# Kernel optimization log

Measured on AMD Instinct MI355X. Metric: run time of the kernel, lower is better.

Reference implementation:

```python
import math
import jax
import jax.numpy as jnp
import numpy as np

WH, WW = 8, 8
DIM, NUM_HEADS = 768, 24
CPB_HIDDEN = 512


def _rel_tables(Wh, Ww):
    # relative_position_index: (N, N) int, values in [0, (2Wh-1)*(2Ww-1))
    coords = np.stack(np.meshgrid(np.arange(Wh), np.arange(Ww), indexing='ij')).reshape(2, -1)
    rel = coords[:, :, None] - coords[:, None, :]          # (2, N, N)
    rel = rel.transpose(1, 2, 0).astype(np.int64)          # (N, N, 2)
    rel[:, :, 0] += Wh - 1
    rel[:, :, 1] += Ww - 1
    rel[:, :, 0] *= 2 * Ww - 1
    idx = rel.sum(-1)                                      # (N, N)
    # relative_coords_table: ((2Wh-1)*(2Ww-1), 2), log-spaced CPB coords
    rch = np.arange(-(Wh - 1), Wh, dtype=np.float32)
    rcw = np.arange(-(Ww - 1), Ww, dtype=np.float32)
    table = np.stack(np.meshgrid(rch, rcw, indexing='ij')).transpose(1, 2, 0).reshape(-1, 2)
    table[:, 0] /= max(Wh - 1, 1)
    table[:, 1] /= max(Ww - 1, 1)
    table *= 8.0
    table = np.sign(table) * np.log2(np.abs(table) + 1.0) / math.log2(8.0)
    return idx.astype(np.int32), table.astype(np.float32)


def setup_inputs() -> dict:
    key = jax.random.key(0)
    ks = jax.random.split(key, 8)
    B_, N, C = 1024, WH * WW, DIM
    idx, table = _rel_tables(WH, WW)
    return {
        'x': jax.random.normal(ks[0], (B_, N, C), dtype=jnp.float32),
        'qkv_w': jax.random.normal(ks[1], (C, 3 * C), dtype=jnp.float32) * 0.02,
        'qkv_b': jnp.zeros((3 * C,), dtype=jnp.float32),
        'proj_w': jax.random.normal(ks[2], (C, C), dtype=jnp.float32) * 0.02,
        'proj_b': jnp.zeros((C,), dtype=jnp.float32),
        'cpb_w1': jax.random.normal(ks[3], (2, CPB_HIDDEN), dtype=jnp.float32) * 0.1,
        'cpb_b1': jnp.zeros((CPB_HIDDEN,), dtype=jnp.float32),
        'cpb_w2': jax.random.normal(ks[4], (CPB_HIDDEN, NUM_HEADS), dtype=jnp.float32) * 0.05,
        'logit_scale': jnp.full((NUM_HEADS, 1, 1), math.log(10.0), dtype=jnp.float32),
        'rel_coords_table': jnp.asarray(table),
        'rel_pos_index': jnp.asarray(idx),
    }


def reference(x, qkv_w, qkv_b, proj_w, proj_b, cpb_w1, cpb_b1, cpb_w2,
              logit_scale, rel_coords_table, rel_pos_index):
    B_, N, C = x.shape
    H = logit_scale.shape[0]
    hd = C // H
    qkv = (x @ qkv_w + qkv_b).reshape(B_, N, 3, H, hd).transpose(2, 0, 3, 1, 4)
    q, k, v = qkv[0], qkv[1], qkv[2]                        # (B_, H, N, hd)
    # cosine attention: L2-normalize q, k (eps as in F.normalize)
    q = q / jnp.maximum(jnp.linalg.norm(q, axis=-1, keepdims=True), 1e-12)
    k = k / jnp.maximum(jnp.linalg.norm(k, axis=-1, keepdims=True), 1e-12)
    ls = jnp.exp(jnp.minimum(logit_scale, math.log(1.0 / 0.01)))  # (H,1,1)
    q = q * ls
    # CPB bias: MLP over rel coords table, gather by relative_position_index
    bias_table = jnp.maximum(rel_coords_table @ cpb_w1 + cpb_b1, 0.0) @ cpb_w2  # (T, H)
    bias = bias_table[rel_pos_index.reshape(-1)].reshape(N, N, H).transpose(2, 0, 1)[None]  # (1,H,N,N)
    attn = jnp.einsum('bhnd,bhmd->bhnm', q, k) + bias      # scale = 1.0
    attn = jax.nn.softmax(attn, axis=-1)
    out = jnp.einsum('bhnm,bhmd->bhnd', attn, v)
    out = out.transpose(0, 2, 1, 3).reshape(B_, N, C)
    return out @ proj_w + proj_b
```

## Files before the change

kernel.cpp:

```cpp
#include <hip/hip_runtime.h>
#include <hip/hip_bf16.h>

typedef __bf16 bf16_t;
typedef __bf16 bf16x8 __attribute__((ext_vector_type(8)));
typedef float f32x4 __attribute__((ext_vector_type(4)));

static __device__ __forceinline__ f32x4 mfma16(bf16x8 a, bf16x8 b, f32x4 c) {
  return __builtin_amdgcn_mfma_f32_16x16x32_bf16(a, b, c, 0, 0, 0);
}

static __device__ __forceinline__ void gload16(const void* g, void* l) {
  __builtin_amdgcn_global_load_lds(
      (const __attribute__((address_space(1))) void*)g,
      (__attribute__((address_space(3))) void*)l, 16, 0, 0);
}

#define BAR() __builtin_amdgcn_s_barrier()
#define SCHED0() __builtin_amdgcn_sched_barrier(0)
#define MEMFENCE() asm volatile("" ::: "memory")
#define BARF() do { BAR(); MEMFENCE(); SCHED0(); } while (0)
#define WAITVM4() do { asm volatile("s_waitcnt vmcnt(4)" ::: "memory"); SCHED0(); } while (0)
#define WAITVM0() do { asm volatile("s_waitcnt vmcnt(0)" ::: "memory"); SCHED0(); } while (0)
#define WAITLGKM0() do { asm volatile("s_waitcnt lgkmcnt(0)" ::: "memory"); SCHED0(); } while (0)
#define SP1 __builtin_amdgcn_s_setprio(1)
#define SP0 __builtin_amdgcn_s_setprio(0)

__global__ __launch_bounds__(256) void cvt_bf16_kernel(
    const float* __restrict__ in, bf16_t* __restrict__ out, int n8) {
  int i = blockIdx.x * 256 + threadIdx.x;
  int stride = gridDim.x * 256;
  for (; i < n8; i += stride) {
    float4 a = ((const float4*)in)[2 * i];
    float4 b = ((const float4*)in)[2 * i + 1];
    bf16x8 w = {(bf16_t)a.x, (bf16_t)a.y, (bf16_t)a.z, (bf16_t)a.w,
                (bf16_t)b.x, (bf16_t)b.y, (bf16_t)b.z, (bf16_t)b.w};
    ((bf16x8*)out)[i] = w;
  }
}

__global__ __launch_bounds__(256) void transpose_cvt_kernel(
    const float* __restrict__ W, bf16_t* __restrict__ WT, int K, int N) {
  __shared__ float tile[32][33];
  int n0 = blockIdx.x * 32, k0 = blockIdx.y * 32;
  int tx = threadIdx.x & 31, ty = threadIdx.x >> 5;
#pragma unroll
  for (int i = 0; i < 32; i += 8)
    tile[ty + i][tx] = W[(size_t)(k0 + ty + i) * N + n0 + tx];
  __syncthreads();
#pragma unroll
  for (int i = 0; i < 32; i += 8)
    WT[(size_t)(n0 + ty + i) * K + k0 + tx] = (bf16_t)tile[tx][ty + i];
}

__global__ __launch_bounds__(512) void cpb_table_kernel(
    const float* __restrict__ table, const float* __restrict__ w1,
    const float* __restrict__ b1, const float* __restrict__ w2,
    float* __restrict__ bias_table) {
  __shared__ float hbuf[512];
  int t = blockIdx.x;
  int j = threadIdx.x;
  float c0 = table[2 * t], c1 = table[2 * t + 1];
  float h = c0 * w1[j] + c1 * w1[512 + j] + b1[j];
  hbuf[j] = h > 0.f ? h : 0.f;
  __syncthreads();
  int wave = j >> 6, lane = j & 63;
  for (int hh = wave * 3; hh < wave * 3 + 3; ++hh) {
    float s = 0.f;
    for (int jj = lane; jj < 512; jj += 64) s += hbuf[jj] * w2[jj * 24 + hh];
    for (int off = 32; off > 0; off >>= 1) s += __shfl_down(s, off, 64);
    if (lane == 0) bias_table[t * 24 + hh] = s;
  }
}

__global__ __launch_bounds__(256) void bias_expand_kernel(
    const float* __restrict__ bias_table, const int* __restrict__ idx,
    float* __restrict__ bias) {
  int h = blockIdx.x;
  for (int nm = threadIdx.x; nm < 4096; nm += 256)
    bias[h * 4096 + nm] = bias_table[idx[nm] * 24 + h];
}

template <int EPI, int NCOLS, int K>
__global__ __launch_bounds__(512, 2) void gemm_kernel(
    const bf16_t* __restrict__ A, const bf16_t* __restrict__ BT,
    const float* __restrict__ bias, void* __restrict__ outp) {
  constexpr int NT = NCOLS / 256;
  constexpr int Kb = K * 2;
  constexpr int nk = K / 64;
  constexpr int nIt = nk / 2;
  __shared__ __align__(16) char lds[131072];
  int tid = threadIdx.x;
  int wave = tid >> 6, lane = tid & 63;
  int wm = wave >> 2, wn = wave & 3;
  int cpx = gridDim.x >> 3;
  int wg = (blockIdx.x & 7) * cpx + (blockIdx.x >> 3);
  int mt = wg / NT, nt = wg % NT;
  int m0 = mt * 256, n0 = nt * 256;

  int srow = tid >> 3;
  int sbc = ((tid & 7) << 4) ^ ((srow & 7) << 4);
  const char* Ag = (const char*)A + (size_t)(m0 + srow) * Kb + sbc;
  const char* Bg = (const char*)BT + (size_t)(n0 + srow) * Kb + sbc;
  char* Al = lds + tid * 16;
  char* Bl = lds + 65536 + tid * 16;

#define ST_A(B_, H_, KT_)                                                     \
  do {                                                                        \
    gload16(Ag + (size_t)((H_) * 128) * Kb + (KT_) * 128,                     \
            Al + (B_) * 32768 + (H_) * 16384);                                \
    gload16(Ag + (size_t)((H_) * 128 + 64) * Kb + (KT_) * 128,                \
            Al + (B_) * 32768 + (H_) * 16384 + 8192);                         \
  } while (0)
#define ST_B(B_, H_, KT_)                                                     \
  do {                                                                        \
    gload16(Bg + (size_t)((H_) * 128) * Kb + (KT_) * 128,                     \
            Bl + (B_) * 32768 + (H_) * 16384);                                \
    gload16(Bg + (size_t)((H_) * 128 + 64) * Kb + (KT_) * 128,                \
            Bl + (B_) * 32768 + (H_) * 16384 + 8192);                         \
  } while (0)

  int r15 = lane & 15, hi = lane >> 4;
  int swz = (lane & 7) << 4;
  int c0 = (hi << 4) ^ swz;
  int c1 = (64 | (hi << 4)) ^ swz;
  const char* aBase = lds + wm * 16384 + r15 * 128;
  const char* bBase = lds + 65536 + (wn >> 1) * 16384 + (wn & 1) * 8192 + r15 * 128;

#define RD_B8(B_)                                                             \
  do {                                                                        \
    _Pragma("unroll") for (int nc = 0; nc < 4; ++nc) {                        \
      bfr[nc][0] = *(const bf16x8*)(bBase + (B_) * 32768 + nc * 2048 + c0);   \
      bfr[nc][1] = *(const bf16x8*)(bBase + (B_) * 32768 + nc * 2048 + c1);   \
    }                                                                         \
  } while (0)
#define RD_A4(B_, MRLO, C_)                                                   \
  do {                                                                        \
    _Pragma("unroll") for (int m_ = 0; m_ < 4; ++m_)                          \
        af[m_] = *(const bf16x8*)(aBase + (B_) * 32768 + ((MRLO) + m_) * 2048 + (C_)); \
  } while (0)
#define MF16(MRLO, KKI)                                                       \
  do {                                                                        \
    _Pragma("unroll") for (int m_ = 0; m_ < 4; ++m_)                          \
        _Pragma("unroll") for (int nc = 0; nc < 4; ++nc)                      \
            acc[(MRLO) + m_][nc] =                                            \
        mfma16(af[m_], bfr[nc][KKI], acc[(MRLO) + m_][nc]);                   \
  } while (0)

  f32x4 acc[8][4] = {};
  ST_B(0, 0, 0); ST_B(0, 1, 0);
  ST_A(0, 0, 0); ST_A(0, 1, 0);
  ST_B(1, 0, 1); ST_B(1, 1, 1);
  WAITVM4();
  BARF();

  for (int it = 0; it < nIt - 1; ++it) {
    int T = 2 * it;
    bf16x8 af[4], bfr[4][2];
    RD_B8(0); RD_A4(0, 0, c0);
    ST_A(1, 0, T + 1); ST_A(1, 1, T + 1);
    BAR(); WAITLGKM0();
    SP1; MF16(0, 0); SP0;
    BARF();
    RD_A4(0, 4, c0);
    ST_B(0, 0, T + 2);
    BAR(); WAITLGKM0();
    SP1; MF16(4, 0); SP0;
    BARF();
    RD_A4(0, 0, c1);
    ST_B(0, 1, T + 2);
    BAR(); WAITLGKM0();
    SP1; MF16(0, 1); SP0;
    BARF();
    RD_A4(0, 4, c1);
    BAR(); WAITLGKM0();
    SP1; MF16(4, 1); SP0;
    WAITVM4();
    BARF();
    RD_B8(1); RD_A4(1, 0, c0);
    ST_A(0, 0, T + 2);
    BAR(); WAITLGKM0();
    SP1; MF16(0, 0); SP0;
    BARF();
    RD_A4(1, 4, c0);
    ST_A(0, 1, T + 2);
    BAR(); WAITLGKM0();
    SP1; MF16(4, 0); SP0;
    BARF();
    RD_A4(1, 0, c1);
    ST_B(1, 0, T + 3);
    BAR(); WAITLGKM0();
    SP1; MF16(0, 1); SP0;
    BARF();
    RD_A4(1, 4, c1);
    ST_B(1, 1, T + 3);
    BAR(); WAITLGKM0();
    SP1; MF16(4, 1); SP0;
    WAITVM4();
    BARF();
  }
  {
    bf16x8 af[4], bfr[4][2];
    RD_B8(0); RD_A4(0, 0, c0);
    ST_A(1, 0, nk - 1); ST_A(1, 1, nk - 1);
    BAR(); WAITLGKM0();
    SP1; MF16(0, 0); SP0;
    BARF();
    RD_A4(0, 4, c0);
    BAR(); WAITLGKM0();
    SP1; MF16(4, 0); SP0;
    BARF();
    RD_A4(0, 0, c1);
    BAR(); WAITLGKM0();
    SP1; MF16(0, 1); SP0;
    BARF();
    RD_A4(0, 4, c1);
    BAR(); WAITLGKM0();
    SP1; MF16(4, 1); SP0;
    WAITVM0();
    BARF();
    RD_B8(1); RD_A4(1, 0, c0);
    BAR(); WAITLGKM0();
    SP1; MF16(0, 0); SP0;
    BARF();
    RD_A4(1, 4, c0);
    BAR(); WAITLGKM0();
    SP1; MF16(4, 0); SP0;
    BARF();
    RD_A4(1, 0, c1);
    BAR(); WAITLGKM0();
    SP1; MF16(0, 1); SP0;
    BARF();
    RD_A4(1, 4, c1);
    BAR(); WAITLGKM0();
    SP1; MF16(4, 1); SP0;
  }

  int hi4 = hi * 4;
  if constexpr (EPI == 0) {
    bf16_t* out = (bf16_t*)outp;
    int sidx = n0 / 768;
#pragma unroll
    for (int mr = 0; mr < 8; ++mr)
#pragma unroll
      for (int nc = 0; nc < 4; ++nc) {
        int gcol = n0 + wn * 64 + nc * 16 + r15;
        int within = gcol - sidx * 768;
        int h = within >> 5, d = within & 31;
        float bv = bias[gcol];
#pragma unroll
        for (int j = 0; j < 4; ++j) {
          int grow = m0 + wm * 128 + mr * 16 + hi4 + j;
          int bwin = grow >> 6, nn = grow & 63;
          size_t off = ((((size_t)sidx * 1024 + bwin) * 24 + h) * 64 + nn) * 32 + d;
          out[off] = (bf16_t)(acc[mr][nc][j] + bv);
        }
      }
  } else {
    float* out = (float*)outp;
#pragma unroll
    for (int mr = 0; mr < 8; ++mr)
#pragma unroll
      for (int nc = 0; nc < 4; ++nc) {
        int gcol = n0 + wn * 64 + nc * 16 + r15;
        float bv = bias[gcol];
#pragma unroll
        for (int j = 0; j < 4; ++j) {
          int grow = m0 + wm * 128 + mr * 16 + hi4 + j;
          out[(size_t)grow * NCOLS + gcol] = acc[mr][nc][j] + bv;
        }
      }
  }
#undef ST_A
#undef ST_B
#undef RD_B8
#undef RD_A4
#undef MF16
}

__global__ __launch_bounds__(64) void attn_kernel(
    const bf16_t* __restrict__ qkv, const float* __restrict__ bias,
    const float* __restrict__ logit_scale, bf16_t* __restrict__ attn_out) {
  __shared__ __align__(16) char smem[14848];
  bf16_t (*qs)[40] = (bf16_t(*)[40])smem;
  bf16_t (*kk)[40] = (bf16_t(*)[40])(smem + 5120);
  bf16_t (*vT)[72] = (bf16_t(*)[72])(smem + 10240);
  bf16_t (*ps)[72] = (bf16_t(*)[72])smem;
  int h = blockIdx.x >> 10;
  int b = blockIdx.x & 1023;
  int lane = threadIdx.x;
  float ls = __expf(fminf(logit_scale[h], 4.6051701859880914f));
  size_t base = ((size_t)b * 24 + h) * 2048;
  const bf16_t* qrow = qkv + base + lane * 32;
  const bf16_t* krow = qkv + (size_t)50331648 + base + lane * 32;
  const bf16_t* vrow = qkv + (size_t)100663296 + base + lane * 32;
  {
    bf16x8 r[4];
#pragma unroll
    for (int i = 0; i < 4; ++i) r[i] = *(const bf16x8*)(qrow + i * 8);
    float f[32], sq = 0.f;
#pragma unroll
    for (int i = 0; i < 4; ++i)
#pragma unroll
      for (int j = 0; j < 8; ++j) { float x = (float)r[i][j]; f[i * 8 + j] = x; sq += x * x; }
    float sc = ls / fmaxf(sqrtf(sq), 1e-12f);
#pragma unroll
    for (int i = 0; i < 4; ++i) {
      bf16x8 w;
#pragma unroll
      for (int j = 0; j < 8; ++j) w[j] = (bf16_t)(f[i * 8 + j] * sc);
      *(bf16x8*)&qs[lane][i * 8] = w;
    }
  }
  {
    bf16x8 r[4];
#pragma unroll
    for (int i = 0; i < 4; ++i) r[i] = *(const bf16x8*)(krow + i * 8);
    float f[32], sq = 0.f;
#pragma unroll
    for (int i = 0; i < 4; ++i)
#pragma unroll
      for (int j = 0; j < 8; ++j) { float x = (float)r[i][j]; f[i * 8 + j] = x; sq += x * x; }
    float sc = 1.f / fmaxf(sqrtf(sq), 1e-12f);
#pragma unroll
    for (int i = 0; i < 4; ++i) {
      bf16x8 w;
#pragma unroll
      for (int j = 0; j < 8; ++j) w[j] = (bf16_t)(f[i * 8 + j] * sc);
      *(bf16x8*)&kk[lane][i * 8] = w;
    }
  }
  {
    bf16x8 r[4];
#pragma unroll
    for (int i = 0; i < 4; ++i) r[i] = *(const bf16x8*)(vrow + i * 8);
#pragma unroll
    for (int i = 0; i < 4; ++i)
#pragma unroll
      for (int j = 0; j < 8; ++j) vT[i * 8 + j][lane] = r[i][j];
  }
  __syncthreads();
  f32x4 sacc[4][4] = {};
  {
    bf16x8 qa[4], kb[4];
#pragma unroll
    for (int mr = 0; mr < 4; ++mr)
      qa[mr] = *(bf16x8*)&qs[mr * 16 + (lane & 15)][(lane >> 4) * 8];
#pragma unroll
    for (int nc = 0; nc < 4; ++nc)
      kb[nc] = *(bf16x8*)&kk[nc * 16 + (lane & 15)][(lane >> 4) * 8];
#pragma unroll
    for (int mr = 0; mr < 4; ++mr)
#pragma unroll
      for (int nc = 0; nc < 4; ++nc)
        sacc[mr][nc] = mfma16(qa[mr], kb[nc], sacc[mr][nc]);
  }
  const float* bh = bias + h * 4096;
  int hi4 = (lane >> 4) * 4;
  float rsum[4][4];
#pragma unroll
  for (int mr = 0; mr < 4; ++mr)
#pragma unroll
    for (int j = 0; j < 4; ++j) {
      int r = mr * 16 + hi4 + j;
      float v0 = __expf(sacc[mr][0][j] + bh[r * 64 + 0 + (lane & 15)]);
      float v1 = __expf(sacc[mr][1][j] + bh[r * 64 + 16 + (lane & 15)]);
      float v2 = __expf(sacc[mr][2][j] + bh[r * 64 + 32 + (lane & 15)]);
      float v3 = __expf(sacc[mr][3][j] + bh[r * 64 + 48 + (lane & 15)]);
      float sum = v0 + v1 + v2 + v3;
#pragma unroll
      for (int off = 1; off < 16; off <<= 1) sum += __shfl_xor(sum, off, 64);
      rsum[mr][j] = sum;
      ps[r][0 + (lane & 15)] = (bf16_t)v0;
      ps[r][16 + (lane & 15)] = (bf16_t)v1;
      ps[r][32 + (lane & 15)] = (bf16_t)v2;
      ps[r][48 + (lane & 15)] = (bf16_t)v3;
    }
  __syncthreads();
  f32x4 oacc[4][2] = {};
#pragma unroll
  for (int ks_ = 0; ks_ < 2; ++ks_) {
    bf16x8 pa[4], vb[2];
#pragma unroll
    for (int mr = 0; mr < 4; ++mr)
      pa[mr] = *(bf16x8*)&ps[mr * 16 + (lane & 15)][ks_ * 32 + (lane >> 4) * 8];
#pragma unroll
    for (int c2 = 0; c2 < 2; ++c2)
      vb[c2] = *(bf16x8*)&vT[c2 * 16 + (lane & 15)][ks_ * 32 + (lane >> 4) * 8];
#pragma unroll
    for (int mr = 0; mr < 4; ++mr)
#pragma unroll
      for (int c2 = 0; c2 < 2; ++c2)
        oacc[mr][c2] = mfma16(pa[mr], vb[c2], oacc[mr][c2]);
  }
#pragma unroll
  for (int mr = 0; mr < 4; ++mr) {
    float rinv[4];
#pragma unroll
    for (int j = 0; j < 4; ++j) rinv[j] = 1.f / rsum[mr][j];
#pragma unroll
    for (int c2 = 0; c2 < 2; ++c2) {
      int d = c2 * 16 + (lane & 15);
#pragma unroll
      for (int j = 0; j < 4; ++j) {
        int r = mr * 16 + hi4 + j;
        attn_out[((size_t)b * 64 + r) * 768 + h * 32 + d] =
            (bf16_t)(oacc[mr][c2][j] * rinv[j]);
      }
    }
  }
}

extern "C" void kernel_launch(void* const* d_in, const int* in_sizes, int n_in,
                              void* d_out, int out_size, void* d_ws, size_t ws_size,
                              hipStream_t stream) {
  const float* x = (const float*)d_in[0];
  const float* qkv_w = (const float*)d_in[1];
  const float* qkv_b = (const float*)d_in[2];
  const float* proj_w = (const float*)d_in[3];
  const float* proj_b = (const float*)d_in[4];
  const float* cpb_w1 = (const float*)d_in[5];
  const float* cpb_b1 = (const float*)d_in[6];
  const float* cpb_w2 = (const float*)d_in[7];
  const float* logit_scale = (const float*)d_in[8];
  const float* rel_tab = (const float*)d_in[9];
  const int* rel_idx = (const int*)d_in[10];

  char* ws = (char*)d_ws;
  float* bias_table = (float*)ws;
  float* bias = (float*)(ws + 32768);
  bf16_t* wTq = (bf16_t*)(ws + 425984);
  bf16_t* wTp = (bf16_t*)(ws + 3964928);
  bf16_t* qkv = (bf16_t*)(ws + 5144576);
  bf16_t* xb = (bf16_t*)(ws + 307134464);
  bf16_t* attn = xb;

  cvt_bf16_kernel<<<2048, 256, 0, stream>>>(x, xb, 6291456);
  transpose_cvt_kernel<<<dim3(72, 24), 256, 0, stream>>>(qkv_w, wTq, 768, 2304);
  transpose_cvt_kernel<<<dim3(24, 24), 256, 0, stream>>>(proj_w, wTp, 768, 768);
  cpb_table_kernel<<<225, 512, 0, stream>>>(rel_tab, cpb_w1, cpb_b1, cpb_w2, bias_table);
  bias_expand_kernel<<<24, 256, 0, stream>>>(bias_table, rel_idx, bias);
  gemm_kernel<0, 2304, 768><<<2304, 512, 0, stream>>>(xb, wTq, qkv_b, qkv);
  attn_kernel<<<24576, 64, 0, stream>>>(qkv, bias, logit_scale, attn);
  gemm_kernel<1, 768, 768><<<768, 512, 0, stream>>>(attn, wTp, proj_b, d_out);
}
```

Before: 538.7 us.

## Double-buffer GEMM LDS fragment reads and shrink attention LDS footprint

Rewrites the GEMM main loop so the LDS fragment reads for the next MFMA group are issued before the current MFMA group runs. It uses two A-fragment and two B-fragment register sets and partial lgkmcnt waits in place of full drains, so LDS read latency overlaps with matrix math. In the attention kernel, V is loaded into registers early and written transposed to LDS only after QK^T, after an extra barrier. This lets vT overlap the q/k region and cuts shared memory per block, which can raise occupancy. The costs are more registers in the GEMM and an extra barrier in attention.

Result: slower. 564.7 us (+4.8%).

```diff
diff --git a/kernel.cpp b/kernel.cpp
--- a/kernel.cpp
+++ b/kernel.cpp
@@ -20,8 +20,11 @@
 #define MEMFENCE() asm volatile("" ::: "memory")
 #define BARF() do { BAR(); MEMFENCE(); SCHED0(); } while (0)
 #define WAITVM4() do { asm volatile("s_waitcnt vmcnt(4)" ::: "memory"); SCHED0(); } while (0)
+#define WAITVM2() do { asm volatile("s_waitcnt vmcnt(2)" ::: "memory"); SCHED0(); } while (0)
 #define WAITVM0() do { asm volatile("s_waitcnt vmcnt(0)" ::: "memory"); SCHED0(); } while (0)
 #define WAITLGKM0() do { asm volatile("s_waitcnt lgkmcnt(0)" ::: "memory"); SCHED0(); } while (0)
+#define WAITLGKM4() do { asm volatile("s_waitcnt lgkmcnt(4)" ::: "memory"); SCHED0(); } while (0)
+#define WAITLGKM12() do { asm volatile("s_waitcnt lgkmcnt(12)" ::: "memory"); SCHED0(); } while (0)
 #define SP1 __builtin_amdgcn_s_setprio(1)
 #define SP0 __builtin_amdgcn_s_setprio(0)
 
@@ -126,113 +129,129 @@
   const char* aBase = lds + wm * 16384 + r15 * 128;
   const char* bBase = lds + 65536 + (wn >> 1) * 16384 + (wn & 1) * 8192 + r15 * 128;
 
-#define RD_B8(B_)                                                             \
+#define RD_B8_TO(DST, B_)                                                     \
   do {                                                                        \
     _Pragma("unroll") for (int nc = 0; nc < 4; ++nc) {                        \
-      bfr[nc][0] = *(const bf16x8*)(bBase + (B_) * 32768 + nc * 2048 + c0);   \
-      bfr[nc][1] = *(const bf16x8*)(bBase + (B_) * 32768 + nc * 2048 + c1);   \
+      DST[nc][0] = *(const bf16x8*)(bBase + (B_) * 32768 + nc * 2048 + c0);   \
+      DST[nc][1] = *(const bf16x8*)(bBase + (B_) * 32768 + nc * 2048 + c1);   \
     }                                                                         \
   } while (0)
-#define RD_A4(B_, MRLO, C_)                                                   \
+#define RD_A4_TO(DST, B_, MRLO, C_)                                           \
   do {                                                                        \
     _Pragma("unroll") for (int m_ = 0; m_ < 4; ++m_)                          \
-        af[m_] = *(const bf16x8*)(aBase + (B_) * 32768 + ((MRLO) + m_) * 2048 + (C_)); \
+        DST[m_] = *(const bf16x8*)(aBase + (B_) * 32768 + ((MRLO) + m_) * 2048 + (C_)); \
   } while (0)
-#define MF16(MRLO, KKI)                                                       \
+#define MF16(MRLO, AF, BF, KKI)                                               \
   do {                                                                        \
     _Pragma("unroll") for (int m_ = 0; m_ < 4; ++m_)                          \
         _Pragma("unroll") for (int nc = 0; nc < 4; ++nc)                      \
             acc[(MRLO) + m_][nc] =                                            \
-        mfma16(af[m_], bfr[nc][KKI], acc[(MRLO) + m_][nc]);                   \
+        mfma16(AF[m_], BF[nc][KKI], acc[(MRLO) + m_][nc]);                    \
   } while (0)
 
   f32x4 acc[8][4] = {};
+  bf16x8 bfr0[4][2], bfr1[4][2], afX[4], afY[4];
+
   ST_B(0, 0, 0); ST_B(0, 1, 0);
   ST_A(0, 0, 0); ST_A(0, 1, 0);
   ST_B(1, 0, 1); ST_B(1, 1, 1);
   WAITVM4();
   BARF();
+  RD_B8_TO(bfr0, 0); RD_A4_TO(afX, 0, 0, c0);
+  SCHED0();
 
   for (int it = 0; it < nIt - 1; ++it) {
     int T = 2 * it;
-    bf16x8 af[4], bfr[4][2];
-    RD_B8(0); RD_A4(0, 0, c0);
+    RD_A4_TO(afY, 0, 4, c0);
+    WAITLGKM4();
+    BAR();
     ST_A(1, 0, T + 1); ST_A(1, 1, T + 1);
-    BAR(); WAITLGKM0();
-    SP1; MF16(0, 0); SP0;
-    BARF();
-    RD_A4(0, 4, c0);
+    SP1; MF16(0, afX, bfr0, 0); SP0;
+    BARF();
+    RD_A4_TO(afX, 0, 0, c1);
+    WAITLGKM4();
+    BAR();
     ST_B(0, 0, T + 2);
-    BAR(); WAITLGKM0();
-    SP1; MF16(4, 0); SP0;
-    BARF();
-    RD_A4(0, 0, c1);
+    SP1; MF16(4, afY, bfr0, 0); SP0;
+    BARF();
+    RD_A4_TO(afY, 0, 4, c1);
+    WAITLGKM4();
+    BAR();
     ST_B(0, 1, T + 2);
-    BAR(); WAITLGKM0();
-    SP1; MF16(0, 1); SP0;
-    BARF();
-    RD_A4(0, 4, c1);
-    BAR(); WAITLGKM0();
-    SP1; MF16(4, 1); SP0;
+    SP1; MF16(0, afX, bfr0, 1); SP0;
     WAITVM4();
     BARF();
-    RD_B8(1); RD_A4(1, 0, c0);
+    RD_B8_TO(bfr1, 1); RD_A4_TO(afX, 1, 0, c0);
+    WAITLGKM12();
+    BAR();
+    SP1; MF16(4, afY, bfr0, 1); SP0;
+    BARF();
+    RD_A4_TO(afY, 1, 4, c0);
+    WAITLGKM4();
+    BAR();
     ST_A(0, 0, T + 2);
-    BAR(); WAITLGKM0();
-    SP1; MF16(0, 0); SP0;
-    BARF();
-    RD_A4(1, 4, c0);
+    SP1; MF16(0, afX, bfr1, 0); SP0;
+    BARF();
+    RD_A4_TO(afX, 1, 0, c1);
+    WAITLGKM4();
+    BAR();
     ST_A(0, 1, T + 2);
-    BAR(); WAITLGKM0();
-    SP1; MF16(4, 0); SP0;
-    BARF();
-    RD_A4(1, 0, c1);
+    SP1; MF16(4, afY, bfr1, 0); SP0;
+    BARF();
+    RD_A4_TO(afY, 1, 4, c1);
+    WAITLGKM4();
+    BAR();
     ST_B(1, 0, T + 3);
-    BAR(); WAITLGKM0();
-    SP1; MF16(0, 1); SP0;
-    BARF();
-    RD_A4(1, 4, c1);
+    SP1; MF16(0, afX, bfr1, 1); SP0;
+    WAITVM2();
+    BARF();
+    RD_B8_TO(bfr0, 0); RD_A4_TO(afX, 0, 0, c0);
+    WAITLGKM12();
+    BAR();
     ST_B(1, 1, T + 3);
-    BAR(); WAITLGKM0();
-    SP1; MF16(4, 1); SP0;
-    WAITVM4();
+    SP1; MF16(4, afY, bfr1, 1); SP0;
     BARF();
   }
   {
-    bf16x8 af[4], bfr[4][2];
-    RD_B8(0); RD_A4(0, 0, c0);
+    RD_A4_TO(afY, 0, 4, c0);
+    WAITLGKM4();
+    BAR();
     ST_A(1, 0, nk - 1); ST_A(1, 1, nk - 1);
-    BAR(); WAITLGKM0();
-    SP1; MF16(0, 0); SP0;
-    BARF();
-    RD_A4(0, 4, c0);
-    BAR(); WAITLGKM0();
-    SP1; MF16(4, 0); SP0;
-    BARF();
-    RD_A4(0, 0, c1);
-    BAR(); WAITLGKM0();
-    SP1; MF16(0, 1); SP0;
-    BARF();
-    RD_A4(0, 4, c1);
-    BAR(); WAITLGKM0();
-    SP1; MF16(4, 1); SP0;
+    SP1; MF16(0, afX, bfr0, 0); SP0;
+    BARF();
+    RD_A4_TO(afX, 0, 0, c1);
+    WAITLGKM4();
+    BAR();
+    SP1; MF16(4, afY, bfr0, 0); SP0;
+    BARF();
+    RD_A4_TO(afY, 0, 4, c1);
+    WAITLGKM4();
+    BAR();
+    SP1; MF16(0, afX, bfr0, 1); SP0;
     WAITVM0();
     BARF();
-    RD_B8(1); RD_A4(1, 0, c0);
-    BAR(); WAITLGKM0();
-    SP1; MF16(0, 0); SP0;
-    BARF();
-    RD_A4(1, 4, c0);
-    BAR(); WAITLGKM0();
-    SP1; MF16(4, 0); SP0;
-    BARF();
-    RD_A4(1, 0, c1);
-    BAR(); WAITLGKM0();
-    SP1; MF16(0, 1); SP0;
-    BARF();
-    RD_A4(1, 4, c1);
-    BAR(); WAITLGKM0();
-    SP1; MF16(4, 1); SP0;
+    RD_B8_TO(bfr1, 1); RD_A4_TO(afX, 1, 0, c0);
+    WAITLGKM12();
+    BAR();
+    SP1; MF16(4, afY, bfr0, 1); SP0;
+    BARF();
+    RD_A4_TO(afY, 1, 4, c0);
+    WAITLGKM4();
+    BAR();
+    SP1; MF16(0, afX, bfr1, 0); SP0;
+    BARF();
+    RD_A4_TO(afX, 1, 0, c1);
+    WAITLGKM4();
+    BAR();
+    SP1; MF16(4, afY, bfr1, 0); SP0;
+    BARF();
+    RD_A4_TO(afY, 1, 4, c1);
+    WAITLGKM4();
+    BAR();
+    SP1; MF16(0, afX, bfr1, 1); SP0;
+    BARF();
+    WAITLGKM0();
+    SP1; MF16(4, afY, bfr1, 1); SP0;
   }
 
   int hi4 = hi * 4;
@@ -272,19 +291,19 @@
   }
 #undef ST_A
 #undef ST_B
-#undef RD_B8
-#undef RD_A4
+#undef RD_B8_TO
+#undef RD_A4_TO
 #undef MF16
 }
 
 __global__ __launch_bounds__(64) void attn_kernel(
     const bf16_t* __restrict__ qkv, const float* __restrict__ bias,
     const float* __restrict__ logit_scale, bf16_t* __restrict__ attn_out) {
-  __shared__ __align__(16) char smem[14848];
+  __shared__ __align__(16) char smem[13824];
   bf16_t (*qs)[40] = (bf16_t(*)[40])smem;
   bf16_t (*kk)[40] = (bf16_t(*)[40])(smem + 5120);
-  bf16_t (*vT)[72] = (bf16_t(*)[72])(smem + 10240);
   bf16_t (*ps)[72] = (bf16_t(*)[72])smem;
+  bf16_t (*vT)[72] = (bf16_t(*)[72])(smem + 9216);
   int h = blockIdx.x >> 10;
   int b = blockIdx.x & 1023;
   int lane = threadIdx.x;
@@ -293,6 +312,9 @@
   const bf16_t* qrow = qkv + base + lane * 32;
   const bf16_t* krow = qkv + (size_t)50331648 + base + lane * 32;
   const bf16_t* vrow = qkv + (size_t)100663296 + base + lane * 32;
+  bf16x8 vreg[4];
+#pragma unroll
+  for (int i = 0; i < 4; ++i) vreg[i] = *(const bf16x8*)(vrow + i * 8);
   {
     bf16x8 r[4];
 #pragma unroll
@@ -328,15 +350,6 @@
       for (int j = 0; j < 8; ++j) w[j] = (bf16_t)(f[i * 8 + j] * sc);
       *(bf16x8*)&kk[lane][i * 8] = w;
     }
-  }
-  {
-    bf16x8 r[4];
-#pragma unroll
-    for (int i = 0; i < 4; ++i) r[i] = *(const bf16x8*)(vrow + i * 8);
-#pragma unroll
-    for (int i = 0; i < 4; ++i)
-#pragma unroll
-      for (int j = 0; j < 8; ++j) vT[i * 8 + j][lane] = r[i][j];
   }
   __syncthreads();
   f32x4 sacc[4][4] = {};
@@ -353,6 +366,13 @@
 #pragma unroll
       for (int nc = 0; nc < 4; ++nc)
         sacc[mr][nc] = mfma16(qa[mr], kb[nc], sacc[mr][nc]);
+  }
+  __syncthreads();
+  {
+#pragma unroll
+    for (int i = 0; i < 4; ++i)
+#pragma unroll
+      for (int j = 0; j < 8; ++j) vT[i * 8 + j][lane] = vreg[i][j];
   }
   const float* bh = bias + h * 4096;
   int hi4 = (lane >> 4) * 4;
```
